# Kernel optimization log

Measured on AMD Instinct MI355X. Metric: run time of the kernel, lower is better.

Reference implementation:

```python
import jax, jax.numpy as jnp
import numpy as np

N_QUBITS = 4
N_LAYERS = 2


def _apply_1q(state, U, w):
    """Apply a single-qubit gate on wire w. state: [B]+[2]*n complex.
    U: [2,2] (shared) or [B,2,2] (per-sample)."""
    s = jnp.moveaxis(state, w + 1, -1)
    if U.ndim == 3:
        s = jnp.einsum('bij,b...j->b...i', U, s)
    else:
        s = jnp.einsum('ij,b...j->b...i', U, s)
    return jnp.moveaxis(s, -1, w + 1)


def _cnot(state, c, t):
    """CNOT with control wire c, target wire t on state [B]+[2]*n."""
    s0 = jnp.take(state, jnp.array([0]), axis=c + 1)
    s1 = jnp.take(state, jnp.array([1]), axis=c + 1)
    s1 = jnp.flip(s1, axis=t + 1)  # X on target when control=1
    return jnp.concatenate([s0, s1], axis=c + 1)


def _rot_matrix(phi, theta, omega):
    """PennyLane Rot(phi,theta,omega) = RZ(omega) RY(theta) RZ(phi)."""
    c = jnp.cos(theta / 2)
    s = jnp.sin(theta / 2)
    ep = jnp.exp(-0.5j * (phi + omega))
    em = jnp.exp(-0.5j * (phi - omega))
    row0 = jnp.stack([ep * c, -jnp.conj(em) * s])
    row1 = jnp.stack([em * s, jnp.conj(ep) * c])
    return jnp.stack([row0, row1]).astype(jnp.complex64)  # [2,2]


def _circuit(x, weights):
    n, L = N_QUBITS, N_LAYERS
    B = x.shape[0]
    angles = jnp.tanh(x[:, :n]) * jnp.float32(np.pi)  # [B, n]
    # |0...0> state, shape [B, 2,2,2,2]
    state = jnp.zeros((B,) + (2,) * n, dtype=jnp.complex64)
    state = state.at[(slice(None),) + (0,) * n].set(1.0)
    # angle encoding: RY(x_i * pi), batched gate per qubit
    for w in range(n):
        th = angles[:, w]
        c = jnp.cos(th / 2)
        s = jnp.sin(th / 2)
        U = jnp.stack([jnp.stack([c, -s], -1),
                       jnp.stack([s, c], -1)], -2).astype(jnp.complex64)  # [B,2,2]
        state = _apply_1q(state, U, w)
    # variational layers
    for l in range(L):
        for w in range(n):
            U = _rot_matrix(weights[l, w, 0], weights[l, w, 1], weights[l, w, 2])
            state = _apply_1q(state, U, w)
        for w in range(n):
            state = _cnot(state, w, (w + 1) % n)
    # <Z_i> for each wire
    probs = state.real ** 2 + state.imag ** 2  # [B]+[2]*n
    outs = []
    for w in range(n):
        p = jnp.moveaxis(probs, w + 1, 1).reshape(B, 2, -1).sum(-1)  # [B,2]
        outs.append(p[:, 0] - p[:, 1])
    return jnp.stack(outs, -1).astype(jnp.float32)  # [B, n]


def setup_inputs() -> dict:
    key = jax.random.key(0)
    k1, k2 = jax.random.split(key)
    x = jax.random.normal(k1, (524288, 8), dtype=jnp.float32)
    weights = jax.random.normal(k2, (N_LAYERS, N_QUBITS, 3), dtype=jnp.float32) * 0.1
    return {"x": x, "weights": weights}


def reference(x, weights):
    return _circuit(x, weights)
```

## Files before the change

kernel.cpp:

```cpp
#include <hip/hip_runtime.h>

#define NQ 4
#define NL 2

__global__ void prep_unitary(const float* __restrict__ w, float* __restrict__ g) {
    int k = threadIdx.x;
    if (k >= 16) return;

    float sr[16], si[16];
#pragma unroll
    for (int j = 0; j < 16; ++j) { sr[j] = 0.f; si[j] = 0.f; }
    sr[k] = 1.f;

#pragma unroll
    for (int l = 0; l < NL; ++l) {
#pragma unroll
        for (int wi = 0; wi < NQ; ++wi) {
            float phi = w[(l * NQ + wi) * 3 + 0];
            float th  = w[(l * NQ + wi) * 3 + 1];
            float om  = w[(l * NQ + wi) * 3 + 2];
            float st, ct, sa, ca, sb, cb;
            sincosf(th * 0.5f, &st, &ct);
            sincosf((phi + om) * 0.5f, &sa, &ca);
            sincosf((phi - om) * 0.5f, &sb, &cb);
            float u00r =  ca * ct, u00i = -sa * ct;
            float u01r = -cb * st, u01i = -sb * st;
            float u10r =  cb * st, u10i = -sb * st;
            float u11r =  ca * ct, u11i =  sa * ct;
            int stb = 8 >> wi;
#pragma unroll
            for (int a = 0; a < 16; ++a) {
                if (a & stb) continue;
                int b = a + stb;
                float ar = sr[a], ai = si[a], br = sr[b], bi = si[b];
                sr[a] = u00r * ar - u00i * ai + u01r * br - u01i * bi;
                si[a] = u00r * ai + u00i * ar + u01r * bi + u01i * br;
                sr[b] = u10r * ar - u10i * ai + u11r * br - u11i * bi;
                si[b] = u10r * ai + u10i * ar + u11r * bi + u11i * br;
            }
        }
#pragma unroll
        for (int c = 0; c < NQ; ++c) {
            int t = (c + 1) & 3, cs = 8 >> c, ts = 8 >> t;
#pragma unroll
            for (int a = 0; a < 16; ++a) {
                if ((a & cs) && !(a & ts)) {
                    int b = a | ts;
                    float tr = sr[a]; sr[a] = sr[b]; sr[b] = tr;
                    float ti = si[a]; si[a] = si[b]; si[b] = ti;
                }
            }
        }
    }

    float* o = g + k * 32;
#pragma unroll
    for (int j = 0; j < 16; ++j) { o[2 * j] = sr[j]; o[2 * j + 1] = si[j]; }
}

__device__ __forceinline__ float fast_tanh(float v) {
    float e = __expf(2.0f * v);
    return 1.0f - 2.0f * __frcp_rn(1.0f + e);
}

__global__ __launch_bounds__(256) void qsim(const float* __restrict__ x,
                                            const float* __restrict__ g,
                                            float* __restrict__ out, int B) {
    int i = blockIdx.x * blockDim.x + threadIdx.x;
    if (i >= B) return;

    float4 xv = *reinterpret_cast<const float4*>(x + (size_t)i * 8);

    const float HALF_PI = 1.57079632679489662f;
    float c[NQ], s[NQ];
    {
        float a;
        a = fast_tanh(xv.x) * HALF_PI; __sincosf(a, &s[0], &c[0]);
        a = fast_tanh(xv.y) * HALF_PI; __sincosf(a, &s[1], &c[1]);
        a = fast_tanh(xv.z) * HALF_PI; __sincosf(a, &s[2], &c[2]);
        a = fast_tanh(xv.w) * HALF_PI; __sincosf(a, &s[3], &c[3]);
    }

    float A[4], Bq[4], s0[16];
#pragma unroll
    for (int a = 0; a < 4; ++a)
        A[a] = ((a & 2) ? s[0] : c[0]) * ((a & 1) ? s[1] : c[1]);
#pragma unroll
    for (int b = 0; b < 4; ++b)
        Bq[b] = ((b & 2) ? s[2] : c[2]) * ((b & 1) ? s[3] : c[3]);
#pragma unroll
    for (int k = 0; k < 16; ++k) s0[k] = A[k >> 2] * Bq[k & 3];

    float2 psi[16];
#pragma unroll
    for (int j = 0; j < 16; ++j) psi[j] = make_float2(0.f, 0.f);

    const float2* G = reinterpret_cast<const float2*>(g);
#pragma unroll
    for (int k = 0; k < 16; ++k) {
        float a = s0[k];
        const float2* col = G + k * 16;
#pragma unroll
        for (int j = 0; j < 16; ++j) {
            float2 u = col[j];
            psi[j].x = fmaf(a, u.x, psi[j].x);
            psi[j].y = fmaf(a, u.y, psi[j].y);
        }
    }

    float p[16];
#pragma unroll
    for (int j = 0; j < 16; ++j)
        p[j] = psi[j].x * psi[j].x + psi[j].y * psi[j].y;

    float4 o = {0.f, 0.f, 0.f, 0.f};
#pragma unroll
    for (int k = 0; k < 16; ++k) {
        o.x += (k & 8) ? -p[k] : p[k];
        o.y += (k & 4) ? -p[k] : p[k];
        o.z += (k & 2) ? -p[k] : p[k];
        o.w += (k & 1) ? -p[k] : p[k];
    }
    *reinterpret_cast<float4*>(out + (size_t)i * 4) = o;
}

extern "C" void kernel_launch(void* const* d_in, const int* in_sizes, int n_in,
                              void* d_out, int out_size, void* d_ws, size_t ws_size,
                              hipStream_t stream) {
    const float* x   = (const float*)d_in[0];
    const float* wts = (const float*)d_in[1];
    float* out       = (float*)d_out;
    float* gates     = (float*)d_ws;

    int B = in_sizes[0] / 8;

    prep_unitary<<<1, 64, 0, stream>>>(wts, gates);

    int threads = 256;
    int blocks  = (B + threads - 1) / threads;
    qsim<<<blocks, threads, 0, stream>>>(x, gates, out, B);
}
```

Measured before the change: 77.76 us.

## Precompute quadratic-form coefficients so per-sample expectation is a symmetric polynomial

The prep kernel now folds the circuit unitary and the Z observables into a 100-entry symmetric quadratic-form coefficient table, exploiting that the encoded input state is real and separable. Each sample then evaluates its four outputs as sums of products of pairwise angle products against that table, replacing the 16x16 complex matrix-vector product and probability reduction. This cuts the per-sample arithmetic and the size of the broadcast table read. The cost is a heavier single-block prep kernel and a precision switch to fast __sincosf for the gate angles.

```diff
diff --git a/kernel.cpp b/kernel.cpp
--- a/kernel.cpp
+++ b/kernel.cpp
@@ -3,60 +3,91 @@
 #define NQ 4
 #define NL 2
 
-__global__ void prep_unitary(const float* __restrict__ w, float* __restrict__ g) {
-    int k = threadIdx.x;
-    if (k >= 16) return;
+__constant__ const int c_PA[10] = {0,0,0,0,1,1,1,2,2,3};
+__constant__ const int c_PB[10] = {0,1,2,3,1,2,3,2,3,3};
 
-    float sr[16], si[16];
+__global__ void prep_coeffs(const float* __restrict__ w, float* __restrict__ g) {
+    __shared__ float Ur[16][16], Ui[16][16];
+    int t = threadIdx.x;
+
+    if (t < 16) {
+        float sr[16], si[16];
 #pragma unroll
-    for (int j = 0; j < 16; ++j) { sr[j] = 0.f; si[j] = 0.f; }
-    sr[k] = 1.f;
+        for (int j = 0; j < 16; ++j) { sr[j] = 0.f; si[j] = 0.f; }
+        sr[t] = 1.f;
 
 #pragma unroll
-    for (int l = 0; l < NL; ++l) {
+        for (int l = 0; l < NL; ++l) {
 #pragma unroll
-        for (int wi = 0; wi < NQ; ++wi) {
-            float phi = w[(l * NQ + wi) * 3 + 0];
-            float th  = w[(l * NQ + wi) * 3 + 1];
-            float om  = w[(l * NQ + wi) * 3 + 2];
-            float st, ct, sa, ca, sb, cb;
-            sincosf(th * 0.5f, &st, &ct);
-            sincosf((phi + om) * 0.5f, &sa, &ca);
-            sincosf((phi - om) * 0.5f, &sb, &cb);
-            float u00r =  ca * ct, u00i = -sa * ct;
-            float u01r = -cb * st, u01i = -sb * st;
-            float u10r =  cb * st, u10i = -sb * st;
-            float u11r =  ca * ct, u11i =  sa * ct;
-            int stb = 8 >> wi;
+            for (int wi = 0; wi < NQ; ++wi) {
+                float phi = w[(l * NQ + wi) * 3 + 0];
+                float th  = w[(l * NQ + wi) * 3 + 1];
+                float om  = w[(l * NQ + wi) * 3 + 2];
+                float st, ct, sa, ca, sb, cb;
+                __sincosf(th * 0.5f, &st, &ct);
+                __sincosf((phi + om) * 0.5f, &sa, &ca);
+                __sincosf((phi - om) * 0.5f, &sb, &cb);
+                float u00r =  ca * ct, u00i = -sa * ct;
+                float u01r = -cb * st, u01i = -sb * st;
+                float u10r =  cb * st, u10i = -sb * st;
+                float u11r =  ca * ct, u11i =  sa * ct;
+                int stb = 8 >> wi;
 #pragma unroll
-            for (int a = 0; a < 16; ++a) {
-                if (a & stb) continue;
-                int b = a + stb;
-                float ar = sr[a], ai = si[a], br = sr[b], bi = si[b];
-                sr[a] = u00r * ar - u00i * ai + u01r * br - u01i * bi;
-                si[a] = u00r * ai + u00i * ar + u01r * bi + u01i * br;
-                sr[b] = u10r * ar - u10i * ai + u11r * br - u11i * bi;
-                si[b] = u10r * ai + u10i * ar + u11r * bi + u11i * br;
+                for (int a = 0; a < 16; ++a) {
+                    if (a & stb) continue;
+                    int b = a + stb;
+                    float ar = sr[a], ai = si[a], br = sr[b], bi = si[b];
+                    sr[a] = u00r * ar - u00i * ai + u01r * br - u01i * bi;
+                    si[a] = u00r * ai + u00i * ar + u01r * bi + u01i * br;
+                    sr[b] = u10r * ar - u10i * ai + u11r * br - u11i * bi;
+                    si[b] = u10r * ai + u10i * ar + u11r * bi + u11i * br;
+                }
+            }
+#pragma unroll
+            for (int c = 0; c < NQ; ++c) {
+                int tt = (c + 1) & 3, cs = 8 >> c, ts = 8 >> tt;
+#pragma unroll
+                for (int a = 0; a < 16; ++a) {
+                    if ((a & cs) && !(a & ts)) {
+                        int b = a | ts;
+                        float tr = sr[a]; sr[a] = sr[b]; sr[b] = tr;
+                        float ti = si[a]; si[a] = si[b]; si[b] = ti;
+                    }
+                }
             }
         }
 #pragma unroll
-        for (int c = 0; c < NQ; ++c) {
-            int t = (c + 1) & 3, cs = 8 >> c, ts = 8 >> t;
-#pragma unroll
-            for (int a = 0; a < 16; ++a) {
-                if ((a & cs) && !(a & ts)) {
-                    int b = a | ts;
-                    float tr = sr[a]; sr[a] = sr[b]; sr[b] = tr;
-                    float ti = si[a]; si[a] = si[b]; si[b] = ti;
-                }
-            }
-        }
+        for (int j = 0; j < 16; ++j) { Ur[j][t] = sr[j]; Ui[j][t] = si[j]; }
     }
 
-    float* o = g + k * 32;
-#pragma unroll
-    for (int j = 0; j < 16; ++j) { o[2 * j] = sr[j]; o[2 * j + 1] = si[j]; }
+    __syncthreads();
+
+    if (t < 100) {
+        int p = t / 10, q = t - p * 10;
+        int a = c_PA[p], a2 = c_PB[p];
+        int b = c_PA[q], b2 = c_PB[q];
+        int k1 = a * 4 + b,  k2 = a2 * 4 + b2;
+        int k3 = a * 4 + b2, k4 = a2 * 4 + b;
+        bool da = (a == a2), db = (b == b2);
+        float m1w = (da && db) ? 1.f : 2.f;
+        float m2w = (!da && !db) ? 2.f : 0.f;
+
+        float acc0 = 0.f, acc1 = 0.f, acc2 = 0.f, acc3 = 0.f;
+        for (int j = 0; j < 16; ++j) {
+            float v1 = Ur[j][k1] * Ur[j][k2] + Ui[j][k1] * Ui[j][k2];
+            float v2 = Ur[j][k3] * Ur[j][k4] + Ui[j][k3] * Ui[j][k4];
+            float v = m1w * v1 + m2w * v2;
+            acc0 += (j & 8) ? -v : v;
+            acc1 += (j & 4) ? -v : v;
+            acc2 += (j & 2) ? -v : v;
+            acc3 += (j & 1) ? -v : v;
+        }
+        float* o = g + t * 4;
+        o[0] = acc0; o[1] = acc1; o[2] = acc2; o[3] = acc3;
+    }
 }
+
+typedef float v4f __attribute__((ext_vector_type(4)));
 
 __device__ __forceinline__ float fast_tanh(float v) {
     float e = __expf(2.0f * v);
@@ -81,47 +112,38 @@
         a = fast_tanh(xv.w) * HALF_PI; __sincosf(a, &s[3], &c[3]);
     }
 
-    float A[4], Bq[4], s0[16];
+    float A[4], Bv[4];
 #pragma unroll
     for (int a = 0; a < 4; ++a)
         A[a] = ((a & 2) ? s[0] : c[0]) * ((a & 1) ? s[1] : c[1]);
 #pragma unroll
     for (int b = 0; b < 4; ++b)
-        Bq[b] = ((b & 2) ? s[2] : c[2]) * ((b & 1) ? s[3] : c[3]);
+        Bv[b] = ((b & 2) ? s[2] : c[2]) * ((b & 1) ? s[3] : c[3]);
+
+    float Aq2[10], Bq2[10];
+    {
+        const int PA[10] = {0,0,0,0,1,1,1,2,2,3};
+        const int PB[10] = {0,1,2,3,1,2,3,2,3,3};
 #pragma unroll
-    for (int k = 0; k < 16; ++k) s0[k] = A[k >> 2] * Bq[k & 3];
-
-    float2 psi[16];
-#pragma unroll
-    for (int j = 0; j < 16; ++j) psi[j] = make_float2(0.f, 0.f);
-
-    const float2* G = reinterpret_cast<const float2*>(g);
-#pragma unroll
-    for (int k = 0; k < 16; ++k) {
-        float a = s0[k];
-        const float2* col = G + k * 16;
-#pragma unroll
-        for (int j = 0; j < 16; ++j) {
-            float2 u = col[j];
-            psi[j].x = fmaf(a, u.x, psi[j].x);
-            psi[j].y = fmaf(a, u.y, psi[j].y);
+        for (int p = 0; p < 10; ++p) {
+            Aq2[p] = A[PA[p]] * A[PB[p]];
+            Bq2[p] = Bv[PA[p]] * Bv[PB[p]];
         }
     }
 
-    float p[16];
+    const v4f* C = reinterpret_cast<const v4f*>(g);
+    v4f acc = {0.f, 0.f, 0.f, 0.f};
 #pragma unroll
-    for (int j = 0; j < 16; ++j)
-        p[j] = psi[j].x * psi[j].x + psi[j].y * psi[j].y;
+    for (int p = 0; p < 10; ++p) {
+        float ap = Aq2[p];
+#pragma unroll
+        for (int q = 0; q < 10; ++q) {
+            float m = ap * Bq2[q];
+            acc += m * C[p * 10 + q];
+        }
+    }
 
-    float4 o = {0.f, 0.f, 0.f, 0.f};
-#pragma unroll
-    for (int k = 0; k < 16; ++k) {
-        o.x += (k & 8) ? -p[k] : p[k];
-        o.y += (k & 4) ? -p[k] : p[k];
-        o.z += (k & 2) ? -p[k] : p[k];
-        o.w += (k & 1) ? -p[k] : p[k];
-    }
-    *reinterpret_cast<float4*>(out + (size_t)i * 4) = o;
+    *reinterpret_cast<v4f*>(out + (size_t)i * 4) = acc;
 }
 
 extern "C" void kernel_launch(void* const* d_in, const int* in_sizes, int n_in,
@@ -130,13 +152,13 @@
     const float* x   = (const float*)d_in[0];
     const float* wts = (const float*)d_in[1];
     float* out       = (float*)d_out;
-    float* gates     = (float*)d_ws;
+    float* coefs     = (float*)d_ws;
 
     int B = in_sizes[0] / 8;
 
-    prep_unitary<<<1, 64, 0, stream>>>(wts, gates);
+    prep_coeffs<<<1, 128, 0, stream>>>(wts, coefs);
 
     int threads = 256;
     int blocks  = (B + threads - 1) / threads;
-    qsim<<<blocks, threads, 0, stream>>>(x, gates, out, B);
+    qsim<<<blocks, threads, 0, stream>>>(x, coefs, out, B);
 }
```

After: 76.02 us. 2.2% less time.
